# Performance work log

Measured on AMD Instinct MI355X. Metric: run time of the kernel, lower is better.

The kernel has to match this reference:

```python
import jax, jax.numpy as jnp
import numpy as np

N_NODES = 100000
N_EDGES = 3200000
IN_EDGE = 2      # input_edge_features_size
IN_NODE = 2      # input_node_features_size
H0 = 10          # hidden_edge_features_sizes[0]
H1 = 10          # hidden_edge_features_sizes[1]
OUT = 2          # output_size of fully_connected_nodes


def _linear_params(key, fan_in, fan_out):
    # torch.nn.Linear default init: U(-1/sqrt(fan_in), 1/sqrt(fan_in))
    k1, k2 = jax.random.split(key)
    bound = 1.0 / np.sqrt(fan_in)
    W = jax.random.uniform(k1, (fan_in, fan_out), minval=-bound, maxval=bound, dtype=jnp.float32)
    b = jax.random.uniform(k2, (fan_out,), minval=-bound, maxval=bound, dtype=jnp.float32)
    return W, b


def setup_inputs() -> dict:
    key = jax.random.key(0)
    ks = jax.random.split(key, 6)
    node_features = jax.random.normal(ks[0], (N_NODES, IN_NODE), dtype=jnp.float32)
    edge_features = jax.random.normal(ks[1], (N_EDGES, IN_EDGE), dtype=jnp.float32)
    edge_index = jax.random.randint(ks[2], (2, N_EDGES), 0, N_NODES, dtype=jnp.int64)
    # fully_connected_edges: Linear(2 -> 10)
    We, be = _linear_params(ks[3], IN_EDGE, H0)
    # DTSP_EdgeUpdate: edge MLP over [edge_feat(10) | src_node(2) | dst_node(2)] -> 10
    Wu, bu = _linear_params(ks[4], H0 + 2 * IN_NODE, H1)
    # fully_connected_nodes: Linear(2 -> 2)
    Wn, bn = _linear_params(ks[5], IN_NODE, OUT)
    return {"node_features": node_features, "edge_features": edge_features,
            "edge_index": edge_index, "We": We, "be": be, "Wu": Wu, "bu": bu,
            "Wn": Wn, "bn": bn}


def reference(node_features, edge_features, edge_index, We, be, Wu, bu, Wn, bn):
    row, col = edge_index[0], edge_index[1]
    # edge_features = self.fully_connected_edges(edge_features)  # [E, 10]
    ef = edge_features @ We + be
    # DTSP_EdgeUpdate: gather endpoint node features per edge, concat, Linear -> [E, 10]
    src = node_features[row]                       # [E, 2] gather
    dst = node_features[col]                       # [E, 2] gather
    ef = jnp.concatenate([ef, src, dst], axis=-1) @ Wu + bu  # [E, 10]
    # Original forward returns only the node branch (edge branch is unused):
    out = node_features @ Wn + bn                  # [N, 2]
    # return both so the gather+MLP edge path is not dead code under jit
    return out, ef
```

## Files before the change

kernel.cpp:

```cpp
#include <hip/hip_runtime.h>

#define N_NODES 100000
#define N_EDGES 3200000

typedef float f4_t __attribute__((ext_vector_type(4)));

__global__ __launch_bounds__(256) void gnn_fused_kernel(
    const float* __restrict__ node, const float* __restrict__ edge,
    const int* __restrict__ ei,
    const float* __restrict__ We, const float* __restrict__ be,
    const float* __restrict__ Wu, const float* __restrict__ bu,
    const float* __restrict__ Wn, const float* __restrict__ bn,
    float* __restrict__ out, float* __restrict__ ef_out)
{
    __shared__ float wf2[80];
    __shared__ int   flagS;
    __shared__ float lds[256 * 21];

    const int tid = threadIdx.x;
    const int t = blockIdx.x * 256 + tid;

    float4 e01 = ((const float4*)edge)[t];

    if (t < N_NODES) {
        float2 nf = ((const float2*)node)[t];
        float o0 = fmaf(nf.y, Wn[2], fmaf(nf.x, Wn[0], bn[0]));
        float o1 = fmaf(nf.y, Wn[3], fmaf(nf.x, Wn[1], bn[1]));
        ((float2*)out)[t] = make_float2(o0, o1);
    }

    if (tid < 60) {
        int r = tid / 10, h = tid % 10;
        float v;
        if (r < 2) {
            v = 0.0f;
            #pragma unroll
            for (int k = 0; k < 10; ++k) v = fmaf(We[r * 10 + k], Wu[k * 10 + h], v);
        } else {
            v = Wu[(10 + (r - 2)) * 10 + h];
        }
        wf2[8 * h + r] = v;
    } else if (tid < 70) {
        int h = tid - 60;
        float v = bu[h];
        #pragma unroll
        for (int k = 0; k < 10; ++k) v = fmaf(be[k], Wu[k * 10 + h], v);
        wf2[8 * h + 6] = v;
    } else if (tid == 70) {
        flagS = (ei[1] == 0 && ei[3] == 0 && ei[5] == 0 && ei[7] == 0) ? 1 : 0;
    }
    __syncthreads();

    const int is64 = flagS;
    int row0, col0, row1, col1;
    if (is64) {
        int4 rr = ((const int4*)ei)[t];
        int4 cc = ((const int4*)(ei + 2 * (size_t)N_EDGES))[t];
        row0 = rr.x; row1 = rr.z; col0 = cc.x; col1 = cc.z;
    } else {
        int2 rr = ((const int2*)ei)[t];
        int2 cc = ((const int2*)(ei + (size_t)N_EDGES))[t];
        row0 = rr.x; row1 = rr.y; col0 = cc.x; col1 = cc.y;
    }

    float2 s0 = ((const float2*)node)[row0];
    float2 d0 = ((const float2*)node)[col0];
    float2 s1 = ((const float2*)node)[row1];
    float2 d1 = ((const float2*)node)[col1];

    float r[20];
    #pragma unroll
    for (int h = 0; h < 10; ++h) {
        const f4_t* wv = (const f4_t*)&wf2[8 * h];
        f4_t wa = wv[0];
        f4_t wb = wv[1];
        float a0 = wb.z, a1 = wb.z;
        a0 = fmaf(e01.x, wa.x, a0);  a1 = fmaf(e01.z, wa.x, a1);
        a0 = fmaf(e01.y, wa.y, a0);  a1 = fmaf(e01.w, wa.y, a1);
        a0 = fmaf(s0.x,  wa.z, a0);  a1 = fmaf(s1.x,  wa.z, a1);
        a0 = fmaf(s0.y,  wa.w, a0);  a1 = fmaf(s1.y,  wa.w, a1);
        a0 = fmaf(d0.x,  wb.x, a0);  a1 = fmaf(d1.x,  wb.x, a1);
        a0 = fmaf(d0.y,  wb.y, a0);  a1 = fmaf(d1.y,  wb.y, a1);
        r[h] = a0; r[10 + h] = a1;
    }

    #pragma unroll
    for (int k = 0; k < 10; ++k) lds[tid * 21 + k] = r[k];
    #pragma unroll
    for (int k = 0; k < 10; ++k) lds[tid * 21 + 10 + k] = r[10 + k];
    __syncthreads();

    f4_t* g4 = (f4_t*)(ef_out + (size_t)blockIdx.x * 5120);
    #pragma unroll
    for (int v = 0; v < 5; ++v) {
        unsigned gidx = v * 256 + tid;
        unsigned p = gidx / 5u;
        unsigned jj = gidx - 5u * p;
        const float* src = &lds[p * 21 + 4 * jj];
        f4_t w = { src[0], src[1], src[2], src[3] };
        __builtin_nontemporal_store(w, &g4[gidx]);
    }
}

extern "C" void kernel_launch(void* const* d_in, const int* in_sizes, int n_in,
                              void* d_out, int out_size, void* d_ws, size_t ws_size,
                              hipStream_t stream) {
    const float* node = (const float*)d_in[0];
    const float* edge = (const float*)d_in[1];
    const int*   ei   = (const int*)d_in[2];
    const float* We   = (const float*)d_in[3];
    const float* be   = (const float*)d_in[4];
    const float* Wu   = (const float*)d_in[5];
    const float* bu   = (const float*)d_in[6];
    const float* Wn   = (const float*)d_in[7];
    const float* bn   = (const float*)d_in[8];

    float* out = (float*)d_out;
    float* ef  = out + 2 * (size_t)N_NODES;

    hipLaunchKernelGGL(gnn_fused_kernel, dim3(N_EDGES / 512), dim3(256), 0, stream,
                       node, edge, ei, We, be, Wu, bu, Wn, bn, out, ef);
}
```

Before: 43.06 us.

## Make each wave independent with per-wave LDS staging and four edges per thread

Replaces block-wide __syncthreads with per-wave LDS staging and wave barriers, so each wavefront builds its own folded weights and transposes its own output. Each thread now handles four edges in two halves, and the grid is halved. This issues more gathers in flight per thread and removes block-level sync stalls. In exchange every wave recomputes the weight fold, and the is64 check is now read by every thread.

```diff
diff --git a/kernel.cpp b/kernel.cpp
--- a/kernel.cpp
+++ b/kernel.cpp
@@ -13,24 +13,47 @@
     const float* __restrict__ Wn, const float* __restrict__ bn,
     float* __restrict__ out, float* __restrict__ ef_out)
 {
-    __shared__ float wf2[80];
-    __shared__ int   flagS;
-    __shared__ float lds[256 * 21];
+    __shared__ float wf[4][80];
+    __shared__ float stg[4][64 * 21];
 
-    const int tid = threadIdx.x;
-    const int t = blockIdx.x * 256 + tid;
+    const int tid   = threadIdx.x;
+    const int lane  = tid & 63;
+    const int wslot = tid >> 6;
+    const int T     = blockIdx.x * 256 + tid;
+    const int gwave = blockIdx.x * 4 + wslot;
+    const size_t E0 = (size_t)gwave * 256;
 
-    float4 e01 = ((const float4*)edge)[t];
+    const bool is64 = (ei[1] == 0) & (ei[3] == 0) & (ei[5] == 0) & (ei[7] == 0);
 
-    if (t < N_NODES) {
-        float2 nf = ((const float2*)node)[t];
+    float4 eA = ((const float4*)edge)[E0 / 2 + lane];
+    float4 eB = ((const float4*)edge)[E0 / 2 + 64 + lane];
+
+    int r0, r1, r2, r3, c0, c1, c2, c3;
+    if (is64) {
+        const int4* R = (const int4*)ei;
+        const int4* C = (const int4*)(ei + 2 * (size_t)N_EDGES);
+        int4 ra = R[E0 / 2 + lane], rb = R[E0 / 2 + 64 + lane];
+        int4 ca = C[E0 / 2 + lane], cb = C[E0 / 2 + 64 + lane];
+        r0 = ra.x; r1 = ra.z; r2 = rb.x; r3 = rb.z;
+        c0 = ca.x; c1 = ca.z; c2 = cb.x; c3 = cb.z;
+    } else {
+        const int2* R = (const int2*)ei;
+        const int2* C = (const int2*)(ei + (size_t)N_EDGES);
+        int2 ra = R[E0 / 2 + lane], rb = R[E0 / 2 + 64 + lane];
+        int2 ca = C[E0 / 2 + lane], cb = C[E0 / 2 + 64 + lane];
+        r0 = ra.x; r1 = ra.y; r2 = rb.x; r3 = rb.y;
+        c0 = ca.x; c1 = ca.y; c2 = cb.x; c3 = cb.y;
+    }
+
+    if (T < N_NODES) {
+        float2 nf = ((const float2*)node)[T];
         float o0 = fmaf(nf.y, Wn[2], fmaf(nf.x, Wn[0], bn[0]));
         float o1 = fmaf(nf.y, Wn[3], fmaf(nf.x, Wn[1], bn[1]));
-        ((float2*)out)[t] = make_float2(o0, o1);
+        ((float2*)out)[T] = make_float2(o0, o1);
     }
 
-    if (tid < 60) {
-        int r = tid / 10, h = tid % 10;
+    if (lane < 60) {
+        int r = lane / 10, h = lane % 10;
         float v;
         if (r < 2) {
             v = 0.0f;
@@ -39,66 +62,86 @@
         } else {
             v = Wu[(10 + (r - 2)) * 10 + h];
         }
-        wf2[8 * h + r] = v;
-    } else if (tid < 70) {
-        int h = tid - 60;
+        wf[wslot][8 * h + r] = v;
+    }
+    if (lane < 10) {
+        int h = lane;
         float v = bu[h];
         #pragma unroll
         for (int k = 0; k < 10; ++k) v = fmaf(be[k], Wu[k * 10 + h], v);
-        wf2[8 * h + 6] = v;
-    } else if (tid == 70) {
-        flagS = (ei[1] == 0 && ei[3] == 0 && ei[5] == 0 && ei[7] == 0) ? 1 : 0;
+        wf[wslot][8 * h + 6] = v;
     }
-    __syncthreads();
+    __builtin_amdgcn_wave_barrier();
 
-    const int is64 = flagS;
-    int row0, col0, row1, col1;
-    if (is64) {
-        int4 rr = ((const int4*)ei)[t];
-        int4 cc = ((const int4*)(ei + 2 * (size_t)N_EDGES))[t];
-        row0 = rr.x; row1 = rr.z; col0 = cc.x; col1 = cc.z;
-    } else {
-        int2 rr = ((const int2*)ei)[t];
-        int2 cc = ((const int2*)(ei + (size_t)N_EDGES))[t];
-        row0 = rr.x; row1 = rr.y; col0 = cc.x; col1 = cc.y;
+    float2 s0 = ((const float2*)node)[r0];
+    float2 d0 = ((const float2*)node)[c0];
+    float2 s1 = ((const float2*)node)[r1];
+    float2 d1 = ((const float2*)node)[c1];
+    float2 s2 = ((const float2*)node)[r2];
+    float2 d2 = ((const float2*)node)[c2];
+    float2 s3 = ((const float2*)node)[r3];
+    float2 d3 = ((const float2*)node)[c3];
+
+    float* S = &stg[wslot][0];
+    const float* WF = &wf[wslot][0];
+    f4_t* g4 = (f4_t*)ef_out + (size_t)gwave * 640;
+
+    {
+        float rr[20];
+        #pragma unroll
+        for (int h = 0; h < 10; ++h) {
+            const f4_t* wv = (const f4_t*)&WF[8 * h];
+            f4_t wa = wv[0];
+            f4_t wb = wv[1];
+            float a0 = wb.z, a1 = wb.z;
+            a0 = fmaf(eA.x, wa.x, a0);  a1 = fmaf(eA.z, wa.x, a1);
+            a0 = fmaf(eA.y, wa.y, a0);  a1 = fmaf(eA.w, wa.y, a1);
+            a0 = fmaf(s0.x, wa.z, a0);  a1 = fmaf(s1.x, wa.z, a1);
+            a0 = fmaf(s0.y, wa.w, a0);  a1 = fmaf(s1.y, wa.w, a1);
+            a0 = fmaf(d0.x, wb.x, a0);  a1 = fmaf(d1.x, wb.x, a1);
+            a0 = fmaf(d0.y, wb.y, a0);  a1 = fmaf(d1.y, wb.y, a1);
+            rr[h] = a0; rr[10 + h] = a1;
+        }
+        #pragma unroll
+        for (int k = 0; k < 20; ++k) S[lane * 21 + k] = rr[k];
+        __builtin_amdgcn_wave_barrier();
+        #pragma unroll
+        for (int v = 0; v < 5; ++v) {
+            unsigned slot = v * 64 + lane;
+            unsigned p = slot / 5u, jj = slot - 5u * p;
+            const float* src = &S[p * 21 + 4 * jj];
+            f4_t w = { src[0], src[1], src[2], src[3] };
+            __builtin_nontemporal_store(w, &g4[slot]);
+        }
+        __builtin_amdgcn_wave_barrier();
     }
-
-    float2 s0 = ((const float2*)node)[row0];
-    float2 d0 = ((const float2*)node)[col0];
-    float2 s1 = ((const float2*)node)[row1];
-    float2 d1 = ((const float2*)node)[col1];
-
-    float r[20];
-    #pragma unroll
-    for (int h = 0; h < 10; ++h) {
-        const f4_t* wv = (const f4_t*)&wf2[8 * h];
-        f4_t wa = wv[0];
-        f4_t wb = wv[1];
-        float a0 = wb.z, a1 = wb.z;
-        a0 = fmaf(e01.x, wa.x, a0);  a1 = fmaf(e01.z, wa.x, a1);
-        a0 = fmaf(e01.y, wa.y, a0);  a1 = fmaf(e01.w, wa.y, a1);
-        a0 = fmaf(s0.x,  wa.z, a0);  a1 = fmaf(s1.x,  wa.z, a1);
-        a0 = fmaf(s0.y,  wa.w, a0);  a1 = fmaf(s1.y,  wa.w, a1);
-        a0 = fmaf(d0.x,  wb.x, a0);  a1 = fmaf(d1.x,  wb.x, a1);
-        a0 = fmaf(d0.y,  wb.y, a0);  a1 = fmaf(d1.y,  wb.y, a1);
-        r[h] = a0; r[10 + h] = a1;
-    }
-
-    #pragma unroll
-    for (int k = 0; k < 10; ++k) lds[tid * 21 + k] = r[k];
-    #pragma unroll
-    for (int k = 0; k < 10; ++k) lds[tid * 21 + 10 + k] = r[10 + k];
-    __syncthreads();
-
-    f4_t* g4 = (f4_t*)(ef_out + (size_t)blockIdx.x * 5120);
-    #pragma unroll
-    for (int v = 0; v < 5; ++v) {
-        unsigned gidx = v * 256 + tid;
-        unsigned p = gidx / 5u;
-        unsigned jj = gidx - 5u * p;
-        const float* src = &lds[p * 21 + 4 * jj];
-        f4_t w = { src[0], src[1], src[2], src[3] };
-        __builtin_nontemporal_store(w, &g4[gidx]);
+    {
+        float rr[20];
+        #pragma unroll
+        for (int h = 0; h < 10; ++h) {
+            const f4_t* wv = (const f4_t*)&WF[8 * h];
+            f4_t wa = wv[0];
+            f4_t wb = wv[1];
+            float a0 = wb.z, a1 = wb.z;
+            a0 = fmaf(eB.x, wa.x, a0);  a1 = fmaf(eB.z, wa.x, a1);
+            a0 = fmaf(eB.y, wa.y, a0);  a1 = fmaf(eB.w, wa.y, a1);
+            a0 = fmaf(s2.x, wa.z, a0);  a1 = fmaf(s3.x, wa.z, a1);
+            a0 = fmaf(s2.y, wa.w, a0);  a1 = fmaf(s3.y, wa.w, a1);
+            a0 = fmaf(d2.x, wb.x, a0);  a1 = fmaf(d3.x, wb.x, a1);
+            a0 = fmaf(d2.y, wb.y, a0);  a1 = fmaf(d3.y, wb.y, a1);
+            rr[h] = a0; rr[10 + h] = a1;
+        }
+        #pragma unroll
+        for (int k = 0; k < 20; ++k) S[lane * 21 + k] = rr[k];
+        __builtin_amdgcn_wave_barrier();
+        #pragma unroll
+        for (int v = 0; v < 5; ++v) {
+            unsigned slot = v * 64 + lane;
+            unsigned p = slot / 5u, jj = slot - 5u * p;
+            const float* src = &S[p * 21 + 4 * jj];
+            f4_t w = { src[0], src[1], src[2], src[3] };
+            __builtin_nontemporal_store(w, &g4[320 + slot]);
+        }
     }
 }
 
@@ -118,6 +161,6 @@
     float* out = (float*)d_out;
     float* ef  = out + 2 * (size_t)N_NODES;
 
-    hipLaunchKernelGGL(gnn_fused_kernel, dim3(N_EDGES / 512), dim3(256), 0, stream,
+    hipLaunchKernelGGL(gnn_fused_kernel, dim3(N_EDGES / 1024), dim3(256), 0, stream,
                        node, edge, ei, We, be, Wu, bu, Wn, bn, out, ef);
 }
```

After: 43.25 us. Within noise of the previous version (+0.4%).
